# Kernel optimization log

Hardware: AMD Instinct MI355X
Metric: run time of the kernel (lower is better)

The kernel has to match this reference:

```python
import jax, jax.numpy as jnp
import numpy as np

N_NODES = 50000
IN_DIM = 64
OUT_DIM = 128
N_EDGES = 800000


def setup_inputs() -> dict:
    key = jax.random.key(0)
    k1, k2, k3, k4, k5 = jax.random.split(key, 5)
    x = jax.random.normal(k1, (N_NODES, IN_DIM), dtype=jnp.float32)
    edge_index = jax.random.randint(k2, (2, N_EDGES), 0, N_NODES, dtype=jnp.int64)
    # PyG SAGEConv params: lin_l (neighbor path, with bias), lin_r (root path, no bias)
    s = 1.0 / np.sqrt(IN_DIM)
    W_l = jax.random.uniform(k3, (OUT_DIM, IN_DIM), dtype=jnp.float32, minval=-s, maxval=s)
    b_l = jax.random.uniform(k4, (OUT_DIM,), dtype=jnp.float32, minval=-s, maxval=s)
    W_r = jax.random.uniform(k5, (OUT_DIM, IN_DIM), dtype=jnp.float32, minval=-s, maxval=s)
    return {"x": x, "edge_index": edge_index, "W_l": W_l, "b_l": b_l, "W_r": W_r}


def reference(x, edge_index, W_l, b_l, W_r):
    # Single-layer GraphSAGE (PyG SAGEConv, mean aggregation).
    # BasicGNN applies no activation after the last (only) layer.
    src = edge_index[0]  # message sources
    dst = edge_index[1]  # aggregation targets
    n = x.shape[0]
    # gather neighbor features and mean-aggregate per destination node
    summed = jax.ops.segment_sum(x[src], dst, num_segments=n)          # [N, IN_DIM]
    cnt = jax.ops.segment_sum(jnp.ones_like(src, dtype=x.dtype), dst, num_segments=n)
    mean = summed / jnp.clip(cnt, 1.0)[:, None]
    # out = lin_l(mean_neighbors) + lin_r(x)
    out = mean @ W_l.T + b_l + x @ W_r.T                               # [N, OUT_DIM]
    return out
```

## Files before the change

kernel.cpp:

```cpp
#include <hip/hip_runtime.h>

#define N_NODES 50000
#define IN_DIM 64
#define OUT_DIM 128
#define N_EDGES 800000

#define NBLK 128
#define EPB (N_EDGES / NBLK)
#define NBUCK 391
#define WLDS 136
#define FIXSCALE 1048576.0f
#define INVFIX (1.0f / 1048576.0f)

typedef __attribute__((ext_vector_type(8))) short bf16x8;
typedef __attribute__((ext_vector_type(4))) float f32x4;

__device__ __forceinline__ unsigned short f2bf(float f) {
    unsigned u = __float_as_uint(f);
    unsigned r = u + 0x7FFFu + ((u >> 16) & 1u);
    return (unsigned short)(r >> 16);
}

__global__ __launch_bounds__(256) void bucket_count_cvt(const int* __restrict__ ei,
                                                        const float* __restrict__ x,
                                                        const float* __restrict__ Wl,
                                                        const float* __restrict__ Wr,
                                                        int* __restrict__ cnt_mat,
                                                        unsigned short* __restrict__ xh,
                                                        unsigned short* __restrict__ w2h)
{
    __shared__ int h[NBUCK];
    int t = threadIdx.x, blk = blockIdx.x;
    for (int i = t; i < NBUCK; i += 256) h[i] = 0;
    __syncthreads();
    int s = blk * EPB;
    for (int i = s + t; i < s + EPB; i += 256)
        atomicAdd(&h[ei[N_EDGES + i] >> 7], 1);
    for (int i = t; i < 6250; i += 256) {
        int gi = blk * 6250 + i;
        float4 v = ((const float4*)x)[gi];
        ushort4 o;
        o.x = f2bf(v.x); o.y = f2bf(v.y); o.z = f2bf(v.z); o.w = f2bf(v.w);
        ((ushort4*)xh)[gi] = o;
    }
    if (t < 64) {
        w2h[blk * 128 + t]      = f2bf(Wr[blk * 64 + t]);
        w2h[blk * 128 + 64 + t] = f2bf(Wl[blk * 64 + t]);
    }
    __syncthreads();
    for (int b = t; b < NBUCK; b += 256) cnt_mat[b * NBLK + blk] = h[b];
}

__global__ __launch_bounds__(256) void rowscan(int* __restrict__ cnt_mat)
{
    __shared__ int tot[NBUCK];
    __shared__ int bst[NBUCK];
    int t = threadIdx.x, lane = t & 63, wid = t >> 6;
    for (int b = t; b < NBUCK; b += 256) {
        const int4* row = (const int4*)(cnt_mat + b * NBLK);
        int sum = 0;
#pragma unroll 8
        for (int i = 0; i < NBLK / 4; ++i) { int4 v = row[i]; sum += v.x + v.y + v.z + v.w; }
        tot[b] = sum;
    }
    __syncthreads();
    if (wid == 0) {
        int carry = 0;
        for (int base = 0; base < NBUCK; base += 64) {
            int i = base + lane;
            int v = (i < NBUCK) ? tot[i] : 0;
            int incl = v;
#pragma unroll
            for (int d = 1; d < 64; d <<= 1) {
                int u = __shfl_up(incl, d, 64);
                if (lane >= d) incl += u;
            }
            if (i < NBUCK) bst[i] = carry + incl - v;
            carry += __shfl(incl, 63, 64);
        }
    }
    __syncthreads();
    int b = blockIdx.x * 4 + wid;
    if (b >= NBUCK) return;
    int base = bst[b];
#pragma unroll
    for (int c = 0; c < 2; ++c) {
        int idx = c * 64 + lane;
        int cv = cnt_mat[b * NBLK + idx];
        int ic = cv;
#pragma unroll
        for (int d = 1; d < 64; d <<= 1) {
            int u = __shfl_up(ic, d, 64);
            if (lane >= d) ic += u;
        }
        cnt_mat[b * NBLK + idx] = base + ic - cv;
        base += __shfl(ic, 63, 64);
    }
}

__global__ __launch_bounds__(256) void bucket_place(const int* __restrict__ ei,
                                                    const int* __restrict__ cnt_scan,
                                                    unsigned* __restrict__ ebuf)
{
    __shared__ int cur[NBUCK];
    int t = threadIdx.x, blk = blockIdx.x;
    for (int b = t; b < NBUCK; b += 256) cur[b] = cnt_scan[b * NBLK + blk];
    __syncthreads();
    int s = blk * EPB;
    for (int i = s + t; i < s + EPB; i += 256) {
        int src = ei[i], dst = ei[N_EDGES + i];
        int slot = atomicAdd(&cur[dst >> 7], 1);
        ebuf[slot] = (unsigned)src | ((unsigned)(dst & 127) << 16);
    }
}

__global__ __launch_bounds__(1024) void gather_mfma(const unsigned short* __restrict__ xh,
                                                    const int* __restrict__ cnt_scan,
                                                    const unsigned* __restrict__ ebuf,
                                                    const unsigned short* __restrict__ w2h,
                                                    const float* __restrict__ bl,
                                                    float* __restrict__ out)
{
    __shared__ int acc[128 * 64];
    __shared__ unsigned short wlds[128 * WLDS];
    __shared__ int dcnt[128];
    __shared__ int range_s[2];
    int t = threadIdx.x, b = blockIdx.x;
    int lane = t & 63, w = t >> 6;

#pragma unroll
    for (int c = 0; c < 2; ++c) {
        int idx = c * 1024 + t;
        int o = idx >> 4, kc = idx & 15;
        bf16x8 v = *(const bf16x8*)(w2h + o * 128 + kc * 8);
        *(bf16x8*)(&wlds[o * WLDS + kc * 8]) = v;
    }
    if (t == 0) {
        range_s[0] = cnt_scan[b * NBLK];
        range_s[1] = (b < NBUCK - 1) ? cnt_scan[(b + 1) * NBLK] : N_EDGES;
    }
#pragma unroll
    for (int i = 0; i < 8; ++i) acc[i * 1024 + t] = 0;
    if (t < 128) dcnt[t] = 0;
    __syncthreads();

    int bs = range_s[0], be = range_s[1];

    for (int e = bs + t; e < be; e += 1024)
        atomicAdd(&dcnt[(ebuf[e] >> 16) & 127], 1);

    for (int e0 = bs + w * 64; e0 < be; e0 += 1024) {
        int m = be - e0; if (m > 64) m = 64;
        unsigned pv = (lane < m) ? ebuf[e0 + lane] : 0u;
        for (int k = 0; k < m; k += 8) {
            unsigned p[8]; int fx[8];
#pragma unroll
            for (int u = 0; u < 8; ++u) p[u] = __shfl(pv, k + u, 64);
#pragma unroll
            for (int u = 0; u < 8; ++u) {
                unsigned short hv = xh[(size_t)(p[u] & 0xFFFFu) * IN_DIM + lane];
                float f = __uint_as_float((unsigned)hv << 16);
                fx[u] = __float2int_rn(f * FIXSCALE);
            }
#pragma unroll
            for (int u = 0; u < 8; ++u)
                if (k + u < m)
                    atomicAdd(&acc[((p[u] >> 16) & 127) * 64 + lane], fx[u]);
        }
    }
    __syncthreads();

    int s_strip = w & 7, hf = w >> 3;
    int nbase = b * 128 + s_strip * 16;
    if (nbase >= N_NODES) return;
    int row = lane & 15, q = lane >> 4;
    int nn = nbase + row;
    size_t nrow = (size_t)((nn < N_NODES) ? nn : (N_NODES - 1));

    bf16x8 a[4];
    a[0] = *(const bf16x8*)(xh + nrow * IN_DIM + q * 8);
    a[1] = *(const bf16x8*)(xh + nrow * IN_DIM + q * 8 + 32);

    int in_node = s_strip * 16 + row;
    int deg = dcnt[in_node];
    float sc = deg ? INVFIX / (float)deg : 0.0f;
    bf16x8 a2, a3;
#pragma unroll
    for (int j = 0; j < 8; ++j) {
        float f0 = (float)acc[in_node * 64 + q * 8 + j] * sc;
        float f1 = (float)acc[in_node * 64 + 32 + q * 8 + j] * sc;
        a2[j] = (short)f2bf(f0);
        a3[j] = (short)f2bf(f1);
    }
    a[2] = a2; a[3] = a3;

    f32x4 accf[4];
#pragma unroll
    for (int jj = 0; jj < 4; ++jj) accf[jj] = (f32x4){0.f, 0.f, 0.f, 0.f};

#pragma unroll
    for (int jj = 0; jj < 4; ++jj) {
        int ot = hf * 4 + jj;
        const unsigned short* wb = &wlds[(ot * 16 + row) * WLDS + q * 8];
#pragma unroll
        for (int s = 0; s < 4; ++s) {
            bf16x8 bfrag = *(const bf16x8*)(wb + s * 32);
            accf[jj] = __builtin_amdgcn_mfma_f32_16x16x32_bf16(a[s], bfrag, accf[jj], 0, 0, 0);
        }
    }

#pragma unroll
    for (int jj = 0; jj < 4; ++jj) {
        int ot = hf * 4 + jj;
        float bias = bl[ot * 16 + row];
#pragma unroll
        for (int r = 0; r < 4; ++r) {
            int n = nbase + q * 4 + r;
            if (n < N_NODES)
                out[(size_t)n * OUT_DIM + ot * 16 + row] = accf[jj][r] + bias;
        }
    }
}

extern "C" void kernel_launch(void* const* d_in, const int* in_sizes, int n_in,
                              void* d_out, int out_size, void* d_ws, size_t ws_size,
                              hipStream_t stream) {
    const float* x  = (const float*)d_in[0];
    const int*   ei = (const int*)d_in[1];
    const float* Wl = (const float*)d_in[2];
    const float* bl = (const float*)d_in[3];
    const float* Wr = (const float*)d_in[4];
    float* out = (float*)d_out;

    int*            cnt_mat = (int*)d_ws;
    unsigned*       ebuf    = (unsigned*)(cnt_mat + NBUCK * NBLK);
    unsigned short* xh      = (unsigned short*)(ebuf + N_EDGES);
    unsigned short* w2h     = xh + (size_t)N_NODES * IN_DIM;

    bucket_count_cvt<<<NBLK, 256, 0, stream>>>(ei, x, Wl, Wr, cnt_mat, xh, w2h);
    rowscan<<<(NBUCK + 3) / 4, 256, 0, stream>>>(cnt_mat);
    bucket_place<<<NBLK, 256, 0, stream>>>(ei, cnt_mat, ebuf);
    gather_mfma<<<NBUCK, 1024, 0, stream>>>(xh, cnt_mat, ebuf, w2h, bl, out);
}
```

Before: 79.14 us.

## Split edges into 1024 partitions, two-kernel scan, swizzle LDS accumulator

Raises the edge partition count from 128 to 1024 blocks for counting and placement so the preprocessing kernels fill the GPU. The scan is split into a per-bucket row-sum kernel and a per-bucket scan kernel to match the larger count matrix. The LDS accumulator in the gather kernel is XOR-swizzled to cut bank conflicts when the per-node rows are read back for the MFMA stage. The cost is an extra kernel launch and a count matrix eight times larger.

```diff
diff --git a/kernel.cpp b/kernel.cpp
--- a/kernel.cpp
+++ b/kernel.cpp
@@ -5,8 +5,8 @@
 #define OUT_DIM 128
 #define N_EDGES 800000
 
-#define NBLK 128
-#define EPB (N_EDGES / NBLK)
+#define NPART 1024
+#define EPP 782
 #define NBUCK 391
 #define WLDS 136
 #define FIXSCALE 1048576.0f
@@ -21,81 +21,96 @@
     return (unsigned short)(r >> 16);
 }
 
-__global__ __launch_bounds__(256) void bucket_count_cvt(const int* __restrict__ ei,
-                                                        const float* __restrict__ x,
-                                                        const float* __restrict__ Wl,
-                                                        const float* __restrict__ Wr,
-                                                        int* __restrict__ cnt_mat,
-                                                        unsigned short* __restrict__ xh,
-                                                        unsigned short* __restrict__ w2h)
+__device__ __forceinline__ int SW(int nd, int f) { return (nd << 6) + (f ^ ((nd & 7) << 3)); }
+
+__global__ __launch_bounds__(256) void p1_count_cvt(const int* __restrict__ ei,
+                                                    const float* __restrict__ x,
+                                                    const float* __restrict__ Wl,
+                                                    const float* __restrict__ Wr,
+                                                    int* __restrict__ cnt_mat,
+                                                    unsigned short* __restrict__ xh,
+                                                    unsigned short* __restrict__ w2h)
 {
     __shared__ int h[NBUCK];
     int t = threadIdx.x, blk = blockIdx.x;
     for (int i = t; i < NBUCK; i += 256) h[i] = 0;
     __syncthreads();
-    int s = blk * EPB;
-    for (int i = s + t; i < s + EPB; i += 256)
+    int s = blk * EPP;
+    int e_end = min(s + EPP, N_EDGES);
+    for (int i = s + t; i < e_end; i += 256)
         atomicAdd(&h[ei[N_EDGES + i] >> 7], 1);
-    for (int i = t; i < 6250; i += 256) {
-        int gi = blk * 6250 + i;
+    for (int gi = blk * 256 + t; gi < N_NODES * 16; gi += NPART * 256) {
         float4 v = ((const float4*)x)[gi];
         ushort4 o;
         o.x = f2bf(v.x); o.y = f2bf(v.y); o.z = f2bf(v.z); o.w = f2bf(v.w);
         ((ushort4*)xh)[gi] = o;
     }
-    if (t < 64) {
+    if (blk < 128 && t < 64) {
         w2h[blk * 128 + t]      = f2bf(Wr[blk * 64 + t]);
         w2h[blk * 128 + 64 + t] = f2bf(Wl[blk * 64 + t]);
     }
     __syncthreads();
-    for (int b = t; b < NBUCK; b += 256) cnt_mat[b * NBLK + blk] = h[b];
-}
-
-__global__ __launch_bounds__(256) void rowscan(int* __restrict__ cnt_mat)
-{
-    __shared__ int tot[NBUCK];
-    __shared__ int bst[NBUCK];
-    int t = threadIdx.x, lane = t & 63, wid = t >> 6;
-    for (int b = t; b < NBUCK; b += 256) {
-        const int4* row = (const int4*)(cnt_mat + b * NBLK);
-        int sum = 0;
-#pragma unroll 8
-        for (int i = 0; i < NBLK / 4; ++i) { int4 v = row[i]; sum += v.x + v.y + v.z + v.w; }
-        tot[b] = sum;
-    }
-    __syncthreads();
-    if (wid == 0) {
+    for (int b = t; b < NBUCK; b += 256) cnt_mat[b * NPART + blk] = h[b];
+}
+
+__global__ __launch_bounds__(256) void rowsum(const int* __restrict__ cnt_mat,
+                                              int* __restrict__ tot)
+{
+    __shared__ int ws[4];
+    int t = threadIdx.x, b = blockIdx.x;
+    int lane = t & 63, w = t >> 6;
+    int4 v = ((const int4*)(cnt_mat + b * NPART))[t];
+    int sv = v.x + v.y + v.z + v.w;
+#pragma unroll
+    for (int d = 32; d >= 1; d >>= 1) sv += __shfl_down(sv, d, 64);
+    if (lane == 0) ws[w] = sv;
+    __syncthreads();
+    if (t == 0) tot[b] = ws[0] + ws[1] + ws[2] + ws[3];
+}
+
+__global__ __launch_bounds__(256) void rowscan2(int* __restrict__ cnt_mat,
+                                                const int* __restrict__ tot)
+{
+    __shared__ int bst_s;
+    __shared__ int wtot[4];
+    int t = threadIdx.x, b = blockIdx.x;
+    int lane = t & 63, w = t >> 6;
+
+    int4 mine = ((const int4*)(cnt_mat + b * NPART))[t];
+    int s = mine.x + mine.y + mine.z + mine.w;
+    int incl = s;
+#pragma unroll
+    for (int d = 1; d < 64; d <<= 1) {
+        int u = __shfl_up(incl, d, 64);
+        if (lane >= d) incl += u;
+    }
+    if (lane == 63) wtot[w] = incl;
+
+    if (w == 0) {
         int carry = 0;
         for (int base = 0; base < NBUCK; base += 64) {
             int i = base + lane;
             int v = (i < NBUCK) ? tot[i] : 0;
-            int incl = v;
+            int ic = v;
 #pragma unroll
             for (int d = 1; d < 64; d <<= 1) {
-                int u = __shfl_up(incl, d, 64);
-                if (lane >= d) incl += u;
+                int u = __shfl_up(ic, d, 64);
+                if (lane >= d) ic += u;
             }
-            if (i < NBUCK) bst[i] = carry + incl - v;
-            carry += __shfl(incl, 63, 64);
-        }
-    }
-    __syncthreads();
-    int b = blockIdx.x * 4 + wid;
-    if (b >= NBUCK) return;
-    int base = bst[b];
-#pragma unroll
-    for (int c = 0; c < 2; ++c) {
-        int idx = c * 64 + lane;
-        int cv = cnt_mat[b * NBLK + idx];
-        int ic = cv;
-#pragma unroll
-        for (int d = 1; d < 64; d <<= 1) {
-            int u = __shfl_up(ic, d, 64);
-            if (lane >= d) ic += u;
-        }
-        cnt_mat[b * NBLK + idx] = base + ic - cv;
-        base += __shfl(ic, 63, 64);
-    }
+            if (i == b) bst_s = carry + ic - v;
+            carry += __shfl(ic, 63, 64);
+        }
+    }
+    __syncthreads();
+    int woff = 0;
+    for (int j = 0; j < w; ++j) woff += wtot[j];
+    int base = bst_s + woff + incl - s;
+    int4 outv;
+    outv.x = base;
+    outv.y = base + mine.x;
+    outv.z = base + mine.x + mine.y;
+    outv.w = base + mine.x + mine.y + mine.z;
+    ((int4*)(cnt_mat + b * NPART))[t] = outv;
 }
 
 __global__ __launch_bounds__(256) void bucket_place(const int* __restrict__ ei,
@@ -104,10 +119,11 @@
 {
     __shared__ int cur[NBUCK];
     int t = threadIdx.x, blk = blockIdx.x;
-    for (int b = t; b < NBUCK; b += 256) cur[b] = cnt_scan[b * NBLK + blk];
-    __syncthreads();
-    int s = blk * EPB;
-    for (int i = s + t; i < s + EPB; i += 256) {
+    for (int b = t; b < NBUCK; b += 256) cur[b] = cnt_scan[b * NPART + blk];
+    __syncthreads();
+    int s = blk * EPP;
+    int e_end = min(s + EPP, N_EDGES);
+    for (int i = s + t; i < e_end; i += 256) {
         int src = ei[i], dst = ei[N_EDGES + i];
         int slot = atomicAdd(&cur[dst >> 7], 1);
         ebuf[slot] = (unsigned)src | ((unsigned)(dst & 127) << 16);
@@ -136,8 +152,8 @@
         *(bf16x8*)(&wlds[o * WLDS + kc * 8]) = v;
     }
     if (t == 0) {
-        range_s[0] = cnt_scan[b * NBLK];
-        range_s[1] = (b < NBUCK - 1) ? cnt_scan[(b + 1) * NBLK] : N_EDGES;
+        range_s[0] = cnt_scan[b * NPART];
+        range_s[1] = (b < NBUCK - 1) ? cnt_scan[(b + 1) * NPART] : N_EDGES;
     }
 #pragma unroll
     for (int i = 0; i < 8; ++i) acc[i * 1024 + t] = 0;
@@ -159,13 +175,12 @@
 #pragma unroll
             for (int u = 0; u < 8; ++u) {
                 unsigned short hv = xh[(size_t)(p[u] & 0xFFFFu) * IN_DIM + lane];
-                float f = __uint_as_float((unsigned)hv << 16);
-                fx[u] = __float2int_rn(f * FIXSCALE);
+                fx[u] = __float2int_rn(__uint_as_float((unsigned)hv << 16) * FIXSCALE);
             }
 #pragma unroll
             for (int u = 0; u < 8; ++u)
                 if (k + u < m)
-                    atomicAdd(&acc[((p[u] >> 16) & 127) * 64 + lane], fx[u]);
+                    atomicAdd(&acc[SW((p[u] >> 16) & 127, lane)], fx[u]);
         }
     }
     __syncthreads();
@@ -187,10 +202,8 @@
     bf16x8 a2, a3;
 #pragma unroll
     for (int j = 0; j < 8; ++j) {
-        float f0 = (float)acc[in_node * 64 + q * 8 + j] * sc;
-        float f1 = (float)acc[in_node * 64 + 32 + q * 8 + j] * sc;
-        a2[j] = (short)f2bf(f0);
-        a3[j] = (short)f2bf(f1);
+        a2[j] = (short)f2bf((float)acc[SW(in_node, q * 8 + j)] * sc);
+        a3[j] = (short)f2bf((float)acc[SW(in_node, 32 + q * 8 + j)] * sc);
     }
     a[2] = a2; a[3] = a3;
 
@@ -233,12 +246,14 @@
     float* out = (float*)d_out;
 
     int*            cnt_mat = (int*)d_ws;
-    unsigned*       ebuf    = (unsigned*)(cnt_mat + NBUCK * NBLK);
+    int*            tot     = cnt_mat + NBUCK * NPART;
+    unsigned*       ebuf    = (unsigned*)(tot + NBUCK + 1);
     unsigned short* xh      = (unsigned short*)(ebuf + N_EDGES);
     unsigned short* w2h     = xh + (size_t)N_NODES * IN_DIM;
 
-    bucket_count_cvt<<<NBLK, 256, 0, stream>>>(ei, x, Wl, Wr, cnt_mat, xh, w2h);
-    rowscan<<<(NBUCK + 3) / 4, 256, 0, stream>>>(cnt_mat);
-    bucket_place<<<NBLK, 256, 0, stream>>>(ei, cnt_mat, ebuf);
+    p1_count_cvt<<<NPART, 256, 0, stream>>>(ei, x, Wl, Wr, cnt_mat, xh, w2h);
+    rowsum<<<NBUCK, 256, 0, stream>>>(cnt_mat, tot);
+    rowscan2<<<NBUCK, 256, 0, stream>>>(cnt_mat, tot);
+    bucket_place<<<NPART, 256, 0, stream>>>(ei, cnt_mat, ebuf);
     gather_mfma<<<NBUCK, 1024, 0, stream>>>(xh, cnt_mat, ebuf, w2h, bl, out);
 }
```

New measurement: 75.04 us. 1.05x faster.
